# Performance work log

Measured on AMD Instinct MI355X. Metric: run time of the kernel, lower is better.

The kernel has to match this reference:

```python
import jax, jax.numpy as jnp
import numpy as np

B, S, H, I, E = 2, 2048, 1024, 4096, 8


def setup_inputs() -> dict:
    key = jax.random.key(0)
    k1, k2, k3, k4 = jax.random.split(key, 4)
    hidden_states = jax.random.normal(k1, (B, S, H), dtype=jnp.float32)
    # router: nn.Linear(H, E, bias=False) -> weight (E, H)
    Wr = jax.random.normal(k2, (E, H), dtype=jnp.float32) * 0.02
    # per-expert MLP: Linear(H,I) weight (I,H); Linear(I,H) weight (H,I); stacked over E
    W1 = jax.random.normal(k3, (E, I, H), dtype=jnp.float32) * 0.02
    W2 = jax.random.normal(k4, (E, H, I), dtype=jnp.float32) * 0.02
    return {"hidden_states": hidden_states, "Wr": Wr, "W1": W1, "W2": W2}


def reference(hidden_states, Wr, W1, W2):
    b, s, h = hidden_states.shape
    n_exp = Wr.shape[0]
    x = hidden_states.reshape(-1, h)                      # (N, H)
    logits = x @ Wr.T                                     # (N, E)
    probs = jax.nn.softmax(logits, axis=-1)               # (N, E)
    # top_k with k == num_experts: sorted probs descending (one-hot mask then
    # covers every expert, so each expert sees every token; expert i's output is
    # weighted by the i-th largest prob, exactly as the torch code does).
    top_probs, _ = jax.lax.top_k(probs, n_exp)            # (N, E)
    hmid = jnp.einsum('nh,eih->nei', x, W1)               # (N, E, I)
    hmid = jax.nn.gelu(hmid, approximate=False)           # exact erf GELU (torch nn.GELU default)
    yexp = jnp.einsum('nei,ehi->neh', hmid, W2)           # (N, E, H)
    out = jnp.einsum('neh,ne->nh', yexp, top_probs)       # weighted combine
    return out.reshape(b, s, h)
```

## Files before the change

### kernel.cpp

```cpp
#include <hip/hip_runtime.h>
#include <hip/hip_bf16.h>

#define NTOK 4096
#define HD   1024
#define ID   4096
#define NE   8
#define LDH  (NE * ID)

typedef float  floatx4 __attribute__((ext_vector_type(4)));
typedef __bf16 bf16x8  __attribute__((ext_vector_type(8)));
typedef unsigned short u16;

__device__ __forceinline__ u16 f2bf(float f) {
    union { float f; unsigned int i; } c; c.f = f;
    return (u16)((c.i + 0x7fffu + ((c.i >> 16) & 1u)) >> 16);
}

__device__ __forceinline__ void async_copy16(u16* lds, const u16* g) {
    __builtin_amdgcn_global_load_lds(
        (const __attribute__((address_space(1))) void*)g,
        (__attribute__((address_space(3))) void*)lds, 16, 0, 0);
}

__device__ __forceinline__ float gelu_fast(float v) {
    const float u = v * (0.7978845608f + 0.0356774081f * v * v);
    const float t = 1.f - 2.f / (__expf(2.f * u) + 1.f);
    return 0.5f * v * (1.f + t);
}

#define FENCE()  asm volatile("" ::: "memory")
#define BAR()    do { FENCE(); __builtin_amdgcn_s_barrier(); FENCE(); } while (0)
#define WAITV4() asm volatile("s_waitcnt vmcnt(4)" ::: "memory")
#define WAITV0() asm volatile("s_waitcnt vmcnt(0)" ::: "memory")
#define WAITL0() asm volatile("s_waitcnt lgkmcnt(0)" ::: "memory")

__global__ __launch_bounds__(256) void convert_kernel(
    const float* __restrict__ src, u16* __restrict__ dst)
{
    const size_t i = ((size_t)blockIdx.x * 256 + threadIdx.x) * 8;
    const float4 a = *(const float4*)(src + i);
    const float4 b = *(const float4*)(src + i + 4);
    ushort4 o0, o1;
    o0.x = f2bf(a.x); o0.y = f2bf(a.y); o0.z = f2bf(a.z); o0.w = f2bf(a.w);
    o1.x = f2bf(b.x); o1.y = f2bf(b.y); o1.z = f2bf(b.z); o1.w = f2bf(b.w);
    *(ushort4*)(dst + i)     = o0;
    *(ushort4*)(dst + i + 4) = o1;
}

__global__ __launch_bounds__(256) void router_kernel(
    const float* __restrict__ x, const float* __restrict__ Wr,
    float* __restrict__ wbuf)
{
    const int n    = blockIdx.x * 4 + (threadIdx.x >> 6);
    const int lane = threadIdx.x & 63;
    const float* xr = x + (size_t)n * HD;
    float acc[NE];
#pragma unroll
    for (int e = 0; e < NE; ++e) acc[e] = 0.f;
    for (int h = lane; h < HD; h += 64) {
        const float xv = xr[h];
#pragma unroll
        for (int e = 0; e < NE; ++e) acc[e] += xv * Wr[e * HD + h];
    }
#pragma unroll
    for (int e = 0; e < NE; ++e) {
        float v = acc[e];
#pragma unroll
        for (int off = 32; off > 0; off >>= 1) v += __shfl_xor(v, off, 64);
        acc[e] = v;
    }
    float mx = acc[0];
#pragma unroll
    for (int e = 1; e < NE; ++e) mx = fmaxf(mx, acc[e]);
    float s = 0.f;
#pragma unroll
    for (int e = 0; e < NE; ++e) { acc[e] = __expf(acc[e] - mx); s += acc[e]; }
    const float inv = 1.f / s;
#pragma unroll
    for (int e = 0; e < NE; ++e) acc[e] *= inv;
#pragma unroll
    for (int i = 0; i < NE - 1; ++i)
#pragma unroll
        for (int j = 0; j < NE - 1 - i; ++j) {
            const float a = acc[j], b = acc[j + 1];
            acc[j] = fmaxf(a, b); acc[j + 1] = fminf(a, b);
        }
    if (lane < NE) wbuf[lane * NTOK + n] = acc[lane];
}

__device__ __forceinline__ void gemm256_tile(
    const u16* __restrict__ A, const u16* __restrict__ B,
    int ldA, int ldB, int K, int rowBase, int colBase,
    u16* As0, u16* As1, u16* Bs0, u16* Bs1,
    floatx4 acc[8][4])
{
    const int t    = threadIdx.x;
    const int w    = t >> 6, lane = t & 63;
    const int wm   = w & 1, wn = w >> 1;
    const int quad = lane >> 4, l15 = lane & 15;

    const int srow   = (w << 4) + (lane >> 2);
    const int schunk = ((lane & 3) ^ ((lane >> 3) & 3)) << 3;
    const u16* gA = A + (size_t)(rowBase + srow) * ldA + schunk;
    const u16* gB = B + (size_t)(colBase + srow) * ldB + schunk;
    const size_t hA = (size_t)128 * ldA, hB = (size_t)128 * ldB;
    u16* lA0 = As0 + w * 512;
    u16* lA1 = As1 + w * 512;
    u16* lB0 = Bs0 + w * 512;
    u16* lB1 = Bs1 + w * 512;

    const int sw = (l15 >> 1) & 3;
    int aoff[8], boff[4];
#pragma unroll
    for (int mi = 0; mi < 8; ++mi)
        aoff[mi] = (wm * 128 + mi * 16 + l15) * 32 + ((quad ^ sw) << 3);
#pragma unroll
    for (int ni = 0; ni < 4; ++ni)
        boff[ni] = (wn * 64 + ni * 16 + l15) * 32 + ((quad ^ sw) << 3);

#define STAGE2(lA, lB, kt) do { const int _ko = (kt) << 5;          \
        async_copy16(lA,        gA + _ko);                          \
        async_copy16(lA + 4096, gA + _ko + hA);                     \
        async_copy16(lB,        gB + _ko);                          \
        async_copy16(lB + 4096, gB + _ko + hB); } while (0)

    const int nkt = K >> 5;
    bf16x8 af[8], bfr[4];
    STAGE2(lA0, lB0, 0);
    STAGE2(lA1, lB1, 1);

#pragma unroll 1
    for (int kt = 0; kt < nkt; kt += 2) {
        WAITV4(); BAR();
#pragma unroll
        for (int mi = 0; mi < 8; ++mi) af[mi] = *(const bf16x8*)(As0 + aoff[mi]);
#pragma unroll
        for (int ni = 0; ni < 4; ++ni) bfr[ni] = *(const bf16x8*)(Bs0 + boff[ni]);
        WAITL0();
        __builtin_amdgcn_s_setprio(1);
#pragma unroll
        for (int mi = 0; mi < 4; ++mi)
#pragma unroll
            for (int ni = 0; ni < 4; ++ni)
                acc[mi][ni] = __builtin_amdgcn_mfma_f32_16x16x32_bf16(
                    af[mi], bfr[ni], acc[mi][ni], 0, 0, 0);
        __builtin_amdgcn_s_setprio(0);
        BAR();
        if (kt + 2 < nkt) STAGE2(lA0, lB0, kt + 2);
        __builtin_amdgcn_s_setprio(1);
#pragma unroll
        for (int mi = 4; mi < 8; ++mi)
#pragma unroll
            for (int ni = 0; ni < 4; ++ni)
                acc[mi][ni] = __builtin_amdgcn_mfma_f32_16x16x32_bf16(
                    af[mi], bfr[ni], acc[mi][ni], 0, 0, 0);
        __builtin_amdgcn_s_setprio(0);
        if (kt + 2 < nkt) { WAITV4(); } else { WAITV0(); }
        BAR();
#pragma unroll
        for (int mi = 0; mi < 8; ++mi) af[mi] = *(const bf16x8*)(As1 + aoff[mi]);
#pragma unroll
        for (int ni = 0; ni < 4; ++ni) bfr[ni] = *(const bf16x8*)(Bs1 + boff[ni]);
        WAITL0();
        __builtin_amdgcn_s_setprio(1);
#pragma unroll
        for (int mi = 0; mi < 4; ++mi)
#pragma unroll
            for (int ni = 0; ni < 4; ++ni)
                acc[mi][ni] = __builtin_amdgcn_mfma_f32_16x16x32_bf16(
                    af[mi], bfr[ni], acc[mi][ni], 0, 0, 0);
        __builtin_amdgcn_s_setprio(0);
        BAR();
        if (kt + 3 < nkt) STAGE2(lA1, lB1, kt + 3);
        __builtin_amdgcn_s_setprio(1);
#pragma unroll
        for (int mi = 4; mi < 8; ++mi)
#pragma unroll
            for (int ni = 0; ni < 4; ++ni)
                acc[mi][ni] = __builtin_amdgcn_mfma_f32_16x16x32_bf16(
                    af[mi], bfr[ni], acc[mi][ni], 0, 0, 0);
        __builtin_amdgcn_s_setprio(0);
    }
#undef STAGE2
}

__global__ __launch_bounds__(512, 2) void gemm1_kernel(
    const u16* __restrict__ X, const u16* __restrict__ W1b,
    const float* __restrict__ wbuf, u16* __restrict__ hmid)
{
    __shared__ __align__(16) u16 As[2][8192];
    __shared__ __align__(16) u16 Bs[2][8192];
    floatx4 acc[8][4] = {};
    const int bid = blockIdx.x;
    const int swz = (bid & 7) * 256 + (bid >> 3);
    const int mt = swz >> 7, nt = swz & 127;
    const int rowBase = mt * 256, colBase = nt * 256;
    const int e = colBase >> 12;

    gemm256_tile(X, W1b, HD, HD, HD, rowBase, colBase,
                 As[0], As[1], Bs[0], Bs[1], acc);

    const int t = threadIdx.x, w = t >> 6, lane = t & 63;
    const int wm = w & 1, wn = w >> 1, quad = lane >> 4, l15 = lane & 15;
#pragma unroll
    for (int mi = 0; mi < 8; ++mi)
#pragma unroll
        for (int r = 0; r < 4; ++r) {
            const int row = rowBase + wm * 128 + mi * 16 + quad * 4 + r;
            const float wv = wbuf[e * NTOK + row];
#pragma unroll
            for (int ni = 0; ni < 4; ++ni) {
                const int col = colBase + wn * 64 + ni * 16 + l15;
                hmid[(size_t)row * LDH + col] =
                    f2bf(gelu_fast(acc[mi][ni][r]) * wv);
            }
        }
}

__global__ __launch_bounds__(512, 2) void gemm2_kernel(
    const u16* __restrict__ hmid, const u16* __restrict__ W2b,
    float* __restrict__ accbuf)
{
    __shared__ __align__(16) u16 As[2][8192];
    __shared__ __align__(16) u16 Bs[2][8192];
    floatx4 acc[8][4] = {};
    const int bid = blockIdx.x;
    const int swz = (bid & 7) * 32 + (bid >> 3);
    const int z = swz >> 6, mt = (swz >> 2) & 15, nt = swz & 3;
    const int rowBase = mt * 256, colBase = nt * 256;

    for (int ee = 0; ee < 2; ++ee) {
        const int e = 2 * z + ee;
        gemm256_tile(hmid + (size_t)e * ID, W2b + (size_t)e * HD * ID,
                     LDH, ID, ID, rowBase, colBase,
                     As[0], As[1], Bs[0], Bs[1], acc);
    }

    float* accs = accbuf + (size_t)z * NTOK * HD;
    const int t = threadIdx.x, w = t >> 6, lane = t & 63;
    const int wm = w & 1, wn = w >> 1, quad = lane >> 4, l15 = lane & 15;
#pragma unroll
    for (int mi = 0; mi < 8; ++mi)
#pragma unroll
        for (int r = 0; r < 4; ++r) {
            const int row = rowBase + wm * 128 + mi * 16 + quad * 4 + r;
#pragma unroll
            for (int ni = 0; ni < 4; ++ni) {
                const int col = colBase + wn * 64 + ni * 16 + l15;
                accs[(size_t)row * HD + col] = acc[mi][ni][r];
            }
        }
}

__global__ __launch_bounds__(256) void finalize_kernel(
    const float* __restrict__ accbuf, float* __restrict__ out)
{
    const size_t NH = (size_t)NTOK * HD;
    const size_t i = ((size_t)blockIdx.x * 256 + threadIdx.x) * 4;
    const float4 a = *(const float4*)(accbuf + i);
    const float4 b = *(const float4*)(accbuf + NH + i);
    const float4 c = *(const float4*)(accbuf + 2 * NH + i);
    const float4 d = *(const float4*)(accbuf + 3 * NH + i);
    float4 o;
    o.x = a.x + b.x + c.x + d.x; o.y = a.y + b.y + c.y + d.y;
    o.z = a.z + b.z + c.z + d.z; o.w = a.w + b.w + c.w + d.w;
    *(float4*)(out + i) = o;
}

extern "C" void kernel_launch(void* const* d_in, const int* in_sizes, int n_in,
                              void* d_out, int out_size, void* d_ws, size_t ws_size,
                              hipStream_t stream) {
    const float* x  = (const float*)d_in[0];
    const float* Wr = (const float*)d_in[1];
    const float* W1 = (const float*)d_in[2];
    const float* W2 = (const float*)d_in[3];
    float* out = (float*)d_out;

    const size_t MB = 1024 * 1024;
    char* ws = (char*)d_ws;
    float* wbuf   = (float*)ws;
    u16*   Xb     = (u16*)(ws + 131072);
    u16*   W1b    = (u16*)(ws + 131072 + 8 * MB);
    u16*   W2b    = (u16*)(ws + 131072 + 72 * MB);
    u16*   hmid   = (u16*)(ws + 131072 + 136 * MB);
    float* accbuf = (float*)(ws + 131072 + 392 * MB);
    if (ws_size < 131072 + 456 * MB) return;

    convert_kernel<<<dim3((NTOK * HD) / 2048), 256, 0, stream>>>(x, Xb);
    convert_kernel<<<dim3((NE * ID * HD) / 2048), 256, 0, stream>>>(W1, W1b);
    convert_kernel<<<dim3((NE * HD * ID) / 2048), 256, 0, stream>>>(W2, W2b);
    router_kernel<<<dim3(NTOK / 4), 256, 0, stream>>>(x, Wr, wbuf);

    gemm1_kernel<<<dim3(NE * ID / 256 * (NTOK / 256)), 512, 0, stream>>>(
        Xb, W1b, wbuf, hmid);
    gemm2_kernel<<<dim3((NTOK / 256) * (HD / 256) * 4), 512, 0, stream>>>(
        hmid, W2b, accbuf);
    finalize_kernel<<<dim3(NTOK * HD / 1024), 256, 0, stream>>>(accbuf, out);
}
```

Before: 974.1 us.

## Switch GEMM mainloop to four-stage LDS ring with prefetch distance three

Replaces the two-buffer ping-pong in the shared bf16 GEMM tile with a four-slot LDS ring, issuing async global->LDS copies three k-steps ahead. Each k-step's copies are split into two halves placed between the MFMA halves, with vmcnt waits adjusted to the deeper queue. The goal is to hide more global memory latency behind MFMA work. In exchange, LDS per block doubles to about 128 KB, which likely allows only one 512-thread block per CU instead of two, and each k-step now has more barriers.

After: 1.016 ms. 4.3% more time.

```diff
diff --git a/kernel.cpp b/kernel.cpp
--- a/kernel.cpp
+++ b/kernel.cpp
@@ -30,6 +30,7 @@
 
 #define FENCE()  asm volatile("" ::: "memory")
 #define BAR()    do { FENCE(); __builtin_amdgcn_s_barrier(); FENCE(); } while (0)
+#define WAITV8() asm volatile("s_waitcnt vmcnt(8)" ::: "memory")
 #define WAITV4() asm volatile("s_waitcnt vmcnt(4)" ::: "memory")
 #define WAITV0() asm volatile("s_waitcnt vmcnt(0)" ::: "memory")
 #define WAITL0() asm volatile("s_waitcnt lgkmcnt(0)" ::: "memory")
@@ -90,12 +91,11 @@
 
 __device__ __forceinline__ void gemm256_tile(
     const u16* __restrict__ A, const u16* __restrict__ B,
-    int ldA, int ldB, int K, int rowBase, int colBase,
-    u16* As0, u16* As1, u16* Bs0, u16* Bs1,
-    floatx4 acc[8][4])
-{
-    const int t    = threadIdx.x;
-    const int w    = t >> 6, lane = t & 63;
+    int ldA, int ldB, int nkt, int rowBase, int colBase,
+    u16* As, u16* Bs, floatx4 acc[8][4])
+{
+    const int tid  = threadIdx.x;
+    const int w    = tid >> 6, lane = tid & 63;
     const int wm   = w & 1, wn = w >> 1;
     const int quad = lane >> 4, l15 = lane & 15;
 
@@ -104,10 +104,7 @@
     const u16* gA = A + (size_t)(rowBase + srow) * ldA + schunk;
     const u16* gB = B + (size_t)(colBase + srow) * ldB + schunk;
     const size_t hA = (size_t)128 * ldA, hB = (size_t)128 * ldB;
-    u16* lA0 = As0 + w * 512;
-    u16* lA1 = As1 + w * 512;
-    u16* lB0 = Bs0 + w * 512;
-    u16* lB1 = Bs1 + w * 512;
+    const int wofs = w << 9;
 
     const int sw = (l15 >> 1) & 3;
     int aoff[8], boff[4];
@@ -118,25 +115,36 @@
     for (int ni = 0; ni < 4; ++ni)
         boff[ni] = (wn * 64 + ni * 16 + l15) * 32 + ((quad ^ sw) << 3);
 
-#define STAGE2(lA, lB, kt) do { const int _ko = (kt) << 5;          \
-        async_copy16(lA,        gA + _ko);                          \
-        async_copy16(lA + 4096, gA + _ko + hA);                     \
-        async_copy16(lB,        gB + _ko);                          \
-        async_copy16(lB + 4096, gB + _ko + hB); } while (0)
-
-    const int nkt = K >> 5;
+#pragma unroll
+    for (int pt = 0; pt < 3; ++pt) {
+        const int ko = pt << 5;
+        u16* lA = As + pt * 8192 + wofs;
+        u16* lB = Bs + pt * 8192 + wofs;
+        async_copy16(lA,        gA + ko);
+        async_copy16(lA + 4096, gA + ko + hA);
+        async_copy16(lB,        gB + ko);
+        async_copy16(lB + 4096, gB + ko + hB);
+    }
+    WAITV8(); BAR();
+
     bf16x8 af[8], bfr[4];
-    STAGE2(lA0, lB0, 0);
-    STAGE2(lA1, lB1, 1);
-
 #pragma unroll 1
-    for (int kt = 0; kt < nkt; kt += 2) {
-        WAITV4(); BAR();
-#pragma unroll
-        for (int mi = 0; mi < 8; ++mi) af[mi] = *(const bf16x8*)(As0 + aoff[mi]);
-#pragma unroll
-        for (int ni = 0; ni < 4; ++ni) bfr[ni] = *(const bf16x8*)(Bs0 + boff[ni]);
-        WAITL0();
+    for (int t = 0; t < nkt; ++t) {
+        const u16* Ab = As + (t & 3) * 8192;
+        const u16* Bb = Bs + (t & 3) * 8192;
+        const int ts = t + 3;
+        u16* sA = As + (ts & 3) * 8192 + wofs;
+        u16* sB = Bs + (ts & 3) * 8192 + wofs;
+        const int ko = ts << 5;
+#pragma unroll
+        for (int mi = 0; mi < 4; ++mi) af[mi] = *(const bf16x8*)(Ab + aoff[mi]);
+#pragma unroll
+        for (int ni = 0; ni < 4; ++ni) bfr[ni] = *(const bf16x8*)(Bb + boff[ni]);
+        if (ts < nkt) {
+            async_copy16(sA, gA + ko);
+            async_copy16(sB, gB + ko);
+        }
+        BAR();
         __builtin_amdgcn_s_setprio(1);
 #pragma unroll
         for (int mi = 0; mi < 4; ++mi)
@@ -146,7 +154,13 @@
                     af[mi], bfr[ni], acc[mi][ni], 0, 0, 0);
         __builtin_amdgcn_s_setprio(0);
         BAR();
-        if (kt + 2 < nkt) STAGE2(lA0, lB0, kt + 2);
+#pragma unroll
+        for (int mi = 4; mi < 8; ++mi) af[mi] = *(const bf16x8*)(Ab + aoff[mi]);
+        if (ts < nkt) {
+            async_copy16(sA + 4096, gA + ko + hA);
+            async_copy16(sB + 4096, gB + ko + hB);
+        }
+        BAR();
         __builtin_amdgcn_s_setprio(1);
 #pragma unroll
         for (int mi = 4; mi < 8; ++mi)
@@ -155,41 +169,20 @@
                 acc[mi][ni] = __builtin_amdgcn_mfma_f32_16x16x32_bf16(
                     af[mi], bfr[ni], acc[mi][ni], 0, 0, 0);
         __builtin_amdgcn_s_setprio(0);
-        if (kt + 2 < nkt) { WAITV4(); } else { WAITV0(); }
-        BAR();
-#pragma unroll
-        for (int mi = 0; mi < 8; ++mi) af[mi] = *(const bf16x8*)(As1 + aoff[mi]);
-#pragma unroll
-        for (int ni = 0; ni < 4; ++ni) bfr[ni] = *(const bf16x8*)(Bs1 + boff[ni]);
         WAITL0();
-        __builtin_amdgcn_s_setprio(1);
-#pragma unroll
-        for (int mi = 0; mi < 4; ++mi)
-#pragma unroll
-            for (int ni = 0; ni < 4; ++ni)
-                acc[mi][ni] = __builtin_amdgcn_mfma_f32_16x16x32_bf16(
-                    af[mi], bfr[ni], acc[mi][ni], 0, 0, 0);
-        __builtin_amdgcn_s_setprio(0);
-        BAR();
-        if (kt + 3 < nkt) STAGE2(lA1, lB1, kt + 3);
-        __builtin_amdgcn_s_setprio(1);
-#pragma unroll
-        for (int mi = 4; mi < 8; ++mi)
-#pragma unroll
-            for (int ni = 0; ni < 4; ++ni)
-                acc[mi][ni] = __builtin_amdgcn_mfma_f32_16x16x32_bf16(
-                    af[mi], bfr[ni], acc[mi][ni], 0, 0, 0);
-        __builtin_amdgcn_s_setprio(0);
-    }
-#undef STAGE2
+        if (t + 4 <= nkt)      { WAITV8(); }
+        else if (t + 3 <= nkt) { WAITV4(); }
+        else                   { WAITV0(); }
+        BAR();
+    }
 }
 
 __global__ __launch_bounds__(512, 2) void gemm1_kernel(
     const u16* __restrict__ X, const u16* __restrict__ W1b,
     const float* __restrict__ wbuf, u16* __restrict__ hmid)
 {
-    __shared__ __align__(16) u16 As[2][8192];
-    __shared__ __align__(16) u16 Bs[2][8192];
+    __shared__ __align__(16) u16 As[4][8192];
+    __shared__ __align__(16) u16 Bs[4][8192];
     floatx4 acc[8][4] = {};
     const int bid = blockIdx.x;
     const int swz = (bid & 7) * 256 + (bid >> 3);
@@ -197,8 +190,8 @@
     const int rowBase = mt * 256, colBase = nt * 256;
     const int e = colBase >> 12;
 
-    gemm256_tile(X, W1b, HD, HD, HD, rowBase, colBase,
-                 As[0], As[1], Bs[0], Bs[1], acc);
+    gemm256_tile(X, W1b, HD, HD, HD / 32, rowBase, colBase,
+                 &As[0][0], &Bs[0][0], acc);
 
     const int t = threadIdx.x, w = t >> 6, lane = t & 63;
     const int wm = w & 1, wn = w >> 1, quad = lane >> 4, l15 = lane & 15;
@@ -221,8 +214,8 @@
     const u16* __restrict__ hmid, const u16* __restrict__ W2b,
     float* __restrict__ accbuf)
 {
-    __shared__ __align__(16) u16 As[2][8192];
-    __shared__ __align__(16) u16 Bs[2][8192];
+    __shared__ __align__(16) u16 As[4][8192];
+    __shared__ __align__(16) u16 Bs[4][8192];
     floatx4 acc[8][4] = {};
     const int bid = blockIdx.x;
     const int swz = (bid & 7) * 32 + (bid >> 3);
@@ -232,8 +225,8 @@
     for (int ee = 0; ee < 2; ++ee) {
         const int e = 2 * z + ee;
         gemm256_tile(hmid + (size_t)e * ID, W2b + (size_t)e * HD * ID,
-                     LDH, ID, ID, rowBase, colBase,
-                     As[0], As[1], Bs[0], Bs[1], acc);
+                     LDH, ID, ID / 32, rowBase, colBase,
+                     &As[0][0], &Bs[0][0], acc);
     }
 
     float* accs = accbuf + (size_t)z * NTOK * HD;
```
